# Kernel tuning notes

Measured on AMD Instinct MI355X. Metric: run time of the kernel, lower is better.

The kernel has to match this reference:

```python
import jax, jax.numpy as jnp
import numpy as np

CHUNK = 32
D_INNER, D_STATE, DT_RANK = 512, 16, 32
B_SZ, L_SEQ = 1, 4096


def _chunked_scan(A_bar, Bu, C, cs=CHUNK):
    # A_bar, Bu: (B, L, D, N); C: (B, L, N)
    Bs, L, D, N = A_bar.shape
    pad = (-L) % cs
    if pad:
        A_bar = jnp.pad(A_bar, ((0, 0), (0, pad), (0, 0), (0, 0)), constant_values=1.0)
        Bu = jnp.pad(Bu, ((0, 0), (0, pad), (0, 0), (0, 0)))
        C = jnp.pad(C, ((0, 0), (0, pad), (0, 0)))
    Lp = L + pad
    nc = Lp // cs
    A_c = A_bar.reshape(Bs, nc, cs, D, N)
    Bu_c = Bu.reshape(Bs, nc, cs, D, N)
    C_c = C.reshape(Bs, nc, cs, N)
    # intra-chunk parallel prefix (log-space cumprod)
    A_cum = jnp.exp(jnp.cumsum(jnp.log(jnp.clip(A_c, 1e-8)), axis=2))
    h_intra = A_cum * jnp.cumsum(Bu_c / jnp.clip(A_cum, 1e-8), axis=2)
    total_A = A_cum[:, :, -1]   # (B, nc, D, N)
    h_last = h_intra[:, :, -1]  # (B, nc, D, N)

    def step(carry, inp):
        tA, hL = inp
        return tA * carry + hL, carry  # emit carry BEFORE update (carry_prev)

    init = jnp.zeros((Bs, D, N), A_bar.dtype)
    _, carry_prev = jax.lax.scan(step, init, (jnp.swapaxes(total_A, 0, 1), jnp.swapaxes(h_last, 0, 1)))
    carry_prev = jnp.swapaxes(carry_prev, 0, 1)  # (B, nc, D, N)
    h_full = h_intra + A_cum * carry_prev[:, :, None]
    y = jnp.einsum('bctdn,bctn->bctd', h_full, C_c).reshape(Bs, Lp, D)
    return y[:, :L]


def _chunked_scan_momentum(A_bar, Bu, C, beta, alpha, cs=CHUNK):
    # v_t = beta*v_{t-1} + alpha*Bu_t  resolved via geometric cumsum trick
    L = A_bar.shape[1]
    powers = jnp.arange(L, dtype=Bu.dtype)
    beta_pow = beta ** powers
    Bu_scaled = alpha * Bu / jnp.clip(beta_pow, 1e-12)[None, :, None, None]
    v_series = beta_pow[None, :, None, None] * jnp.cumsum(Bu_scaled, axis=1)
    return _chunked_scan(A_bar, v_series, C, cs)


def setup_inputs() -> dict:
    key = jax.random.key(0)
    ks = jax.random.split(key, 5)
    x = jax.random.normal(ks[0], (B_SZ, L_SEQ, D_INNER), dtype=jnp.float32)
    W_xp = jax.random.normal(ks[1], (DT_RANK + 2 * D_STATE, D_INNER), dtype=jnp.float32) * 0.02
    W_dt = jax.random.normal(ks[2], (D_INNER, DT_RANK), dtype=jnp.float32) * 0.05
    # torch dt bias init: dt ~ exp(U(log1e-3, log1e-1)); bias = log(exp(dt)-1)
    u = jax.random.uniform(ks[3], (D_INNER,), dtype=jnp.float32)
    dt_init = jnp.exp(u * (np.log(0.1) - np.log(0.001)) + np.log(0.001))
    b_dt = jnp.log(jnp.expm1(dt_init))
    A_log = jnp.broadcast_to(jnp.log(jnp.arange(1, D_STATE + 1, dtype=jnp.float32))[None, :], (D_INNER, D_STATE)).copy()
    D_param = jnp.ones((D_INNER,), dtype=jnp.float32)
    alpha = jnp.float32(0.6)
    beta_logit = jnp.float32(np.log(0.99 / (1.0 - 0.99 + 1e-8)))
    return {"x": x, "W_xp": W_xp, "W_dt": W_dt, "b_dt": b_dt, "A_log": A_log,
            "D_param": D_param, "alpha": alpha, "beta_logit": beta_logit}


def reference(x, W_xp, W_dt, b_dt, A_log, D_param, alpha, beta_logit):
    # x: (B, L, d_inner)
    proj = x @ W_xp.T                                   # (B, L, dt_rank + 2N)
    dt_in, Bp, Cp = jnp.split(proj, [DT_RANK, DT_RANK + D_STATE], axis=-1)
    dt = jax.nn.softplus(dt_in @ W_dt.T + b_dt)          # (B, L, D)
    A = -jnp.exp(A_log)                                  # (D, N)
    A_bar = jnp.exp(dt[..., None] * A[None, None])       # (B, L, D, N)
    Bu = dt[..., None] * Bp[:, :, None, :] * x[..., None]  # (B, L, D, N)
    beta = jax.nn.sigmoid(beta_logit)
    y = _chunked_scan_momentum(A_bar, Bu, Cp, beta, alpha, CHUNK)
    return y + D_param * x
```

## Files before the change

kernel.cpp:

```cpp
#include <hip/hip_runtime.h>
#include <math.h>

#define L_SEQ   4096
#define D_INNER 512
#define D_STATE 16
#define DT_RANK 32
#define CHUNK   32
#define NCHUNK  128
#define NCH     8192
#define LN_1EM8 -18.420681f

__global__ __launch_bounds__(256) void k1_proj(
    const float* __restrict__ x, const float* __restrict__ W_xp,
    const float* __restrict__ W_dt, const float* __restrict__ b_dt,
    float* __restrict__ dt_out, float* __restrict__ Bp, float* __restrict__ Cp)
{
    __shared__ __align__(16) float xs[32][36];
    __shared__ __align__(16) float wsd[64][36];
    __shared__ __align__(16) float dtin[32][36];

    const int tid = threadIdx.x;
    const int t0  = blockIdx.x * 32;

    float acc[2][4] = {{0.f,0.f,0.f,0.f},{0.f,0.f,0.f,0.f}};
    const int rt = (tid & 15) * 2;
    const int ct = (tid >> 4) * 4;

    for (int kc = 0; kc < D_INNER; kc += 32) {
        {
            int r  = tid >> 3;
            int k4 = (tid & 7) << 2;
            *(float4*)&xs[r][k4] =
                *(const float4*)&x[(size_t)(t0 + r) * D_INNER + kc + k4];
        }
        #pragma unroll
        for (int i = 0; i < 2; ++i) {
            int e   = tid + i * 256;
            int ccw = e >> 3;
            int kw  = (e & 7) << 2;
            *(float4*)&wsd[ccw][kw] =
                *(const float4*)&W_xp[(size_t)ccw * D_INNER + kc + kw];
        }
        __syncthreads();

        #pragma unroll
        for (int k = 0; k < 32; k += 4) {
            float4 x0 = *(const float4*)&xs[rt][k];
            float4 x1 = *(const float4*)&xs[rt + 1][k];
            float4 w0 = *(const float4*)&wsd[ct][k];
            float4 w1 = *(const float4*)&wsd[ct + 1][k];
            float4 w2 = *(const float4*)&wsd[ct + 2][k];
            float4 w3 = *(const float4*)&wsd[ct + 3][k];
            acc[0][0] += x0.x*w0.x + x0.y*w0.y + x0.z*w0.z + x0.w*w0.w;
            acc[0][1] += x0.x*w1.x + x0.y*w1.y + x0.z*w1.z + x0.w*w1.w;
            acc[0][2] += x0.x*w2.x + x0.y*w2.y + x0.z*w2.z + x0.w*w2.w;
            acc[0][3] += x0.x*w3.x + x0.y*w3.y + x0.z*w3.z + x0.w*w3.w;
            acc[1][0] += x1.x*w0.x + x1.y*w0.y + x1.z*w0.z + x1.w*w0.w;
            acc[1][1] += x1.x*w1.x + x1.y*w1.y + x1.z*w1.z + x1.w*w1.w;
            acc[1][2] += x1.x*w2.x + x1.y*w2.y + x1.z*w2.z + x1.w*w2.w;
            acc[1][3] += x1.x*w3.x + x1.y*w3.y + x1.z*w3.z + x1.w*w3.w;
        }
        __syncthreads();
    }

    #pragma unroll
    for (int rr = 0; rr < 2; ++rr) {
        #pragma unroll
        for (int cj = 0; cj < 4; ++cj) {
            int cc = ct + cj, r = rt + rr;
            float a = acc[rr][cj];
            if (cc < DT_RANK)               dtin[r][cc] = a;
            else if (cc < DT_RANK + D_STATE) Bp[(size_t)(t0 + r) * D_STATE + (cc - DT_RANK)] = a;
            else                             Cp[(size_t)(t0 + r) * D_STATE + (cc - DT_RANK - D_STATE)] = a;
        }
    }
    __syncthreads();

    const int dA = tid * 2, dB = tid * 2 + 1;
    float4 wa[8], wb[8];
    #pragma unroll
    for (int q = 0; q < 8; ++q) {
        wa[q] = *(const float4*)&W_dt[(size_t)dA * DT_RANK + q * 4];
        wb[q] = *(const float4*)&W_dt[(size_t)dB * DT_RANK + q * 4];
    }
    const float bA = b_dt[dA], bB = b_dt[dB];
    for (int r = 0; r < 32; ++r) {
        float zA = bA, zB = bB;
        #pragma unroll
        for (int q = 0; q < 8; ++q) {
            float4 dn = *(const float4*)&dtin[r][q * 4];
            zA += dn.x*wa[q].x + dn.y*wa[q].y + dn.z*wa[q].z + dn.w*wa[q].w;
            zB += dn.x*wb[q].x + dn.y*wb[q].y + dn.z*wb[q].z + dn.w*wb[q].w;
        }
        float2 o;
        o.x = fmaxf(zA, 0.f) + log1pf(expf(-fabsf(zA)));
        o.y = fmaxf(zB, 0.f) + log1pf(expf(-fabsf(zB)));
        *(float2*)&dt_out[(size_t)(t0 + r) * D_INNER + dA] = o;
    }
}

__global__ __launch_bounds__(256) void k2a(
    const float* __restrict__ x, const float* __restrict__ dt,
    const float* __restrict__ Bp, const float* __restrict__ A_log,
    const float* __restrict__ alpha_p, const float* __restrict__ beta_logit_p,
    float4* __restrict__ GTUW)
{
    __shared__ __align__(16) float xs_t[16][36], dts_t[16][36], Bs_t[16][36];
    __shared__ __align__(16) float bpw[32], aib[32];
    const int tid = threadIdx.x;
    const int c   = blockIdx.x;
    const int d0  = blockIdx.y * 16;

    #pragma unroll
    for (int i = 0; i < 2; ++i) {
        int e = tid + i * 256;
        int t = e >> 4, q = e & 15;
        xs_t [q][t] = x [(size_t)(c * CHUNK + t) * D_INNER + d0 + q];
        dts_t[q][t] = dt[(size_t)(c * CHUNK + t) * D_INNER + d0 + q];
        Bs_t [q][t] = Bp[(size_t)(c * CHUNK + t) * D_STATE + q];
    }
    if (tid < CHUNK) {
        float betaf = 1.f / (1.f + expf(-beta_logit_p[0]));
        double lb = log((double)betaf);
        float bp = (float)exp((double)(c * CHUNK + tid) * lb);
        bpw[tid] = bp;
        aib[tid] = alpha_p[0] / fmaxf(bp, 1e-12f);
    }
    __syncthreads();

    const int dl = tid >> 4, n = tid & 15;
    const float A = -expf(A_log[(d0 + dl) * D_STATE + n]);

    float LS = 0.f, csum = 0.f, P1 = 0.f, P2 = 0.f;
    #pragma unroll
    for (int j = 0; j < CHUNK; j += 4) {
        float4 dt4 = *(const float4*)&dts_t[dl][j];
        float4 xx4 = *(const float4*)&xs_t [dl][j];
        float4 BB4 = *(const float4*)&Bs_t [n][j];
        float4 bp4 = *(const float4*)&bpw[j];
        float4 ai4 = *(const float4*)&aib[j];
        #pragma unroll
        for (int u = 0; u < 4; ++u) {
            float dtv = ((const float*)&dt4)[u];
            float xv  = ((const float*)&xx4)[u];
            float Bv  = ((const float*)&BB4)[u];
            float bp  = ((const float*)&bp4)[u];
            float ai  = ((const float*)&ai4)[u];
            float Bu  = dtv * Bv * xv;
            LS   = fmaf(ai, Bu, LS);
            csum = fmaf(dtv, A, csum);
            float rA = (csum < LN_1EM8) ? 1e8f : __expf(-csum);
            float t1 = bp * rA;
            P1 = fmaf(t1, LS, P1);
            P2 += t1;
        }
    }
    float TA = __expf(csum);
    float4 o; o.x = LS; o.y = TA; o.z = TA * P1; o.w = TA * P2;
    GTUW[(size_t)c * NCH + d0 * D_STATE + tid] = o;
}

__global__ __launch_bounds__(64) void k2b(
    const float4* __restrict__ GTUW, float2* __restrict__ SC)
{
    const int ch = blockIdx.x * 64 + threadIdx.x;
    double Soff = 0.0, carry = 0.0;
    for (int c = 0; c < NCHUNK; ++c) {
        const size_t idx = (size_t)c * NCH + ch;
        float2 sc; sc.x = (float)Soff; sc.y = (float)carry;
        SC[idx] = sc;
        float4 g = GTUW[idx];
        carry = (double)g.y * carry + (double)g.z + Soff * (double)g.w;
        Soff += (double)g.x;
    }
}

__global__ __launch_bounds__(256) void k2c(
    const float* __restrict__ x, const float* __restrict__ dt,
    const float* __restrict__ Bp, const float* __restrict__ Cp,
    const float* __restrict__ A_log, const float* __restrict__ D_param,
    const float* __restrict__ alpha_p, const float* __restrict__ beta_logit_p,
    const float2* __restrict__ SC, float* __restrict__ out)
{
    __shared__ __align__(16) float xs_t[16][36], dts_t[16][36];
    __shared__ __align__(16) float Bs_t[16][36], Cs_t[16][36];
    __shared__ __align__(16) float bpw[32], aib[32];
    __shared__ __align__(16) float ys2[CHUNK * 16][20];
    const int tid = threadIdx.x;
    const int c   = blockIdx.x;
    const int d0  = blockIdx.y * 16;

    #pragma unroll
    for (int i = 0; i < 2; ++i) {
        int e = tid + i * 256;
        int t = e >> 4, q = e & 15;
        xs_t [q][t] = x [(size_t)(c * CHUNK + t) * D_INNER + d0 + q];
        dts_t[q][t] = dt[(size_t)(c * CHUNK + t) * D_INNER + d0 + q];
        Bs_t [q][t] = Bp[(size_t)(c * CHUNK + t) * D_STATE + q];
        Cs_t [q][t] = Cp[(size_t)(c * CHUNK + t) * D_STATE + q];
    }
    if (tid < CHUNK) {
        float betaf = 1.f / (1.f + expf(-beta_logit_p[0]));
        double lb = log((double)betaf);
        float bp = (float)exp((double)(c * CHUNK + tid) * lb);
        bpw[tid] = bp;
        aib[tid] = alpha_p[0] / fmaxf(bp, 1e-12f);
    }
    __syncthreads();

    const int dl = tid >> 4, n = tid & 15;
    const float A = -expf(A_log[(d0 + dl) * D_STATE + n]);

    float2 sc = SC[(size_t)c * NCH + d0 * D_STATE + tid];
    const float Soff = sc.x, cprev = sc.y;

    float LS = 0.f, csum = 0.f, P = 0.f;
    #pragma unroll
    for (int j = 0; j < CHUNK; j += 4) {
        float4 dt4 = *(const float4*)&dts_t[dl][j];
        float4 xx4 = *(const float4*)&xs_t [dl][j];
        float4 BB4 = *(const float4*)&Bs_t [n][j];
        float4 CC4 = *(const float4*)&Cs_t [n][j];
        float4 bp4 = *(const float4*)&bpw[j];
        float4 ai4 = *(const float4*)&aib[j];
        #pragma unroll
        for (int u = 0; u < 4; ++u) {
            float dtv = ((const float*)&dt4)[u];
            float xv  = ((const float*)&xx4)[u];
            float Bv  = ((const float*)&BB4)[u];
            float Cv  = ((const float*)&CC4)[u];
            float bp  = ((const float*)&bp4)[u];
            float ai  = ((const float*)&ai4)[u];
            float Bu  = dtv * Bv * xv;
            LS   = fmaf(ai, Bu, LS);
            float v = bp * (Soff + LS);
            csum = fmaf(dtv, A, csum);
            float Acum = __expf(csum);
            float rA = (csum < LN_1EM8) ? 1e8f : __expf(-csum);
            P = fmaf(v, rA, P);
            float hf = Acum * (P + cprev);
            ys2[(j + u) * 16 + dl][n] = hf * Cv;
        }
    }
    __syncthreads();

    #pragma unroll
    for (int i = 0; i < 2; ++i) {
        int p  = tid + i * 256;
        int j  = p >> 4, dl2 = p & 15;
        const float* row = ys2[p];
        float4 a0 = ((const float4*)row)[0];
        float4 a1 = ((const float4*)row)[1];
        float4 a2 = ((const float4*)row)[2];
        float4 a3 = ((const float4*)row)[3];
        float s = a0.x+a0.y+a0.z+a0.w + a1.x+a1.y+a1.z+a1.w
                + a2.x+a2.y+a2.z+a2.w + a3.x+a3.y+a3.z+a3.w;
        int gd = d0 + dl2;
        out[(size_t)(c * CHUNK + j) * D_INNER + gd] = s + D_param[gd] * xs_t[dl2][j];
    }
}

extern "C" void kernel_launch(void* const* d_in, const int* in_sizes, int n_in,
                              void* d_out, int out_size, void* d_ws, size_t ws_size,
                              hipStream_t stream)
{
    const float* x          = (const float*)d_in[0];
    const float* W_xp       = (const float*)d_in[1];
    const float* W_dt       = (const float*)d_in[2];
    const float* b_dt       = (const float*)d_in[3];
    const float* A_log      = (const float*)d_in[4];
    const float* D_param    = (const float*)d_in[5];
    const float* alpha      = (const float*)d_in[6];
    const float* beta_logit = (const float*)d_in[7];
    float* out = (float*)d_out;

    float* ws = (float*)d_ws;
    float*  dt   = ws;
    float*  Bp   = dt + (size_t)L_SEQ * D_INNER;
    float*  Cp   = Bp + (size_t)L_SEQ * D_STATE;
    float4* GTUW = (float4*)(Cp + (size_t)L_SEQ * D_STATE);
    float2* SC   = (float2*)((float*)GTUW + (size_t)4 * NCHUNK * NCH);

    k1_proj<<<L_SEQ / 32, 256, 0, stream>>>(x, W_xp, W_dt, b_dt, dt, Bp, Cp);
    k2a<<<dim3(NCHUNK, D_INNER / 16), 256, 0, stream>>>(
        x, dt, Bp, A_log, alpha, beta_logit, GTUW);
    k2b<<<NCH / 64, 64, 0, stream>>>(GTUW, SC);
    k2c<<<dim3(NCHUNK, D_INNER / 16), 256, 0, stream>>>(
        x, dt, Bp, Cp, A_log, D_param, alpha, beta_logit, SC, out);
}
```

Measured before the change: 169.2 us.

## Split-K projection GEMM, widen scan tiles, prefetch carry scan, shuffle-reduce output

The projection is split into a split-K GEMM over 8 K-slices with a 4x4 register tile, followed by a reduction kernel that also computes dt, B and C. The scan kernels now handle 64 channels per block with 4 states per thread, coalesced row loads and a shuffle reduction over states, instead of a large shared staging buffer. The sequential carry kernel prefetches GTUW four chunks ahead to hide load latency. The cost is one extra launch and a partial-sum buffer that shares workspace with SC, plus fewer blocks in the scan kernels.

```diff
diff --git a/kernel.cpp b/kernel.cpp
--- a/kernel.cpp
+++ b/kernel.cpp
@@ -10,71 +10,81 @@
 #define NCH     8192
 #define LN_1EM8 -18.420681f
 
-__global__ __launch_bounds__(256) void k1_proj(
+__global__ __launch_bounds__(256) void k1a(
     const float* __restrict__ x, const float* __restrict__ W_xp,
-    const float* __restrict__ W_dt, const float* __restrict__ b_dt,
-    float* __restrict__ dt_out, float* __restrict__ Bp, float* __restrict__ Cp)
-{
-    __shared__ __align__(16) float xs[32][36];
-    __shared__ __align__(16) float wsd[64][36];
-    __shared__ __align__(16) float dtin[32][36];
-
+    float* __restrict__ proj_part)
+{
+    __shared__ __align__(16) float xs_t[64][68];
+    __shared__ __align__(16) float ws_t[64][68];
     const int tid = threadIdx.x;
-    const int t0  = blockIdx.x * 32;
-
-    float acc[2][4] = {{0.f,0.f,0.f,0.f},{0.f,0.f,0.f,0.f}};
-    const int rt = (tid & 15) * 2;
-    const int ct = (tid >> 4) * 4;
-
-    for (int kc = 0; kc < D_INNER; kc += 32) {
-        {
-            int r  = tid >> 3;
-            int k4 = (tid & 7) << 2;
-            *(float4*)&xs[r][k4] =
-                *(const float4*)&x[(size_t)(t0 + r) * D_INNER + kc + k4];
+    const int t0  = blockIdx.x * 64;
+    const int k0  = blockIdx.y * 64;
+
+    #pragma unroll
+    for (int i = 0; i < 4; ++i) {
+        int e = tid + i * 256;
+        int r = e >> 4, k4 = (e & 15) << 2;
+        float4 v = *(const float4*)&x[(size_t)(t0 + r) * D_INNER + k0 + k4];
+        xs_t[k4 + 0][r] = v.x; xs_t[k4 + 1][r] = v.y;
+        xs_t[k4 + 2][r] = v.z; xs_t[k4 + 3][r] = v.w;
+        float4 w = *(const float4*)&W_xp[(size_t)r * D_INNER + k0 + k4];
+        ws_t[k4 + 0][r] = w.x; ws_t[k4 + 1][r] = w.y;
+        ws_t[k4 + 2][r] = w.z; ws_t[k4 + 3][r] = w.w;
+    }
+    __syncthreads();
+
+    const int tr = (tid & 15) << 2;
+    const int tc = (tid >> 4) << 2;
+    float a00=0,a01=0,a02=0,a03=0, a10=0,a11=0,a12=0,a13=0;
+    float a20=0,a21=0,a22=0,a23=0, a30=0,a31=0,a32=0,a33=0;
+
+    #pragma unroll 4
+    for (int k = 0; k < 64; ++k) {
+        float4 xv = *(const float4*)&xs_t[k][tr];
+        float4 wv = *(const float4*)&ws_t[k][tc];
+        a00 = fmaf(xv.x, wv.x, a00); a01 = fmaf(xv.x, wv.y, a01);
+        a02 = fmaf(xv.x, wv.z, a02); a03 = fmaf(xv.x, wv.w, a03);
+        a10 = fmaf(xv.y, wv.x, a10); a11 = fmaf(xv.y, wv.y, a11);
+        a12 = fmaf(xv.y, wv.z, a12); a13 = fmaf(xv.y, wv.w, a13);
+        a20 = fmaf(xv.z, wv.x, a20); a21 = fmaf(xv.z, wv.y, a21);
+        a22 = fmaf(xv.z, wv.z, a22); a23 = fmaf(xv.z, wv.w, a23);
+        a30 = fmaf(xv.w, wv.x, a30); a31 = fmaf(xv.w, wv.y, a31);
+        a32 = fmaf(xv.w, wv.z, a32); a33 = fmaf(xv.w, wv.w, a33);
+    }
+    float* base = proj_part + (size_t)blockIdx.y * (L_SEQ * 64);
+    float4 o;
+    o.x=a00; o.y=a01; o.z=a02; o.w=a03; *(float4*)&base[(t0+tr+0)*64 + tc] = o;
+    o.x=a10; o.y=a11; o.z=a12; o.w=a13; *(float4*)&base[(t0+tr+1)*64 + tc] = o;
+    o.x=a20; o.y=a21; o.z=a22; o.w=a23; *(float4*)&base[(t0+tr+2)*64 + tc] = o;
+    o.x=a30; o.y=a31; o.z=a32; o.w=a33; *(float4*)&base[(t0+tr+3)*64 + tc] = o;
+}
+
+__global__ __launch_bounds__(256) void k1b(
+    const float* __restrict__ proj_part, const float* __restrict__ W_dt,
+    const float* __restrict__ b_dt, float* __restrict__ dt_out,
+    float* __restrict__ Bp, float* __restrict__ Cp)
+{
+    __shared__ __align__(16) float ps[16][68];
+    const int tid = threadIdx.x;
+    const int t0  = blockIdx.x * 16;
+
+    {
+        const int r = tid >> 4, q = (tid & 15) << 2;
+        float4 s = {0.f, 0.f, 0.f, 0.f};
+        #pragma unroll
+        for (int p = 0; p < 8; ++p) {
+            float4 v = *(const float4*)&proj_part[(size_t)p * (L_SEQ * 64) + (t0 + r) * 64 + q];
+            s.x += v.x; s.y += v.y; s.z += v.z; s.w += v.w;
         }
-        #pragma unroll
-        for (int i = 0; i < 2; ++i) {
-            int e   = tid + i * 256;
-            int ccw = e >> 3;
-            int kw  = (e & 7) << 2;
-            *(float4*)&wsd[ccw][kw] =
-                *(const float4*)&W_xp[(size_t)ccw * D_INNER + kc + kw];
-        }
-        __syncthreads();
-
-        #pragma unroll
-        for (int k = 0; k < 32; k += 4) {
-            float4 x0 = *(const float4*)&xs[rt][k];
-            float4 x1 = *(const float4*)&xs[rt + 1][k];
-            float4 w0 = *(const float4*)&wsd[ct][k];
-            float4 w1 = *(const float4*)&wsd[ct + 1][k];
-            float4 w2 = *(const float4*)&wsd[ct + 2][k];
-            float4 w3 = *(const float4*)&wsd[ct + 3][k];
-            acc[0][0] += x0.x*w0.x + x0.y*w0.y + x0.z*w0.z + x0.w*w0.w;
-            acc[0][1] += x0.x*w1.x + x0.y*w1.y + x0.z*w1.z + x0.w*w1.w;
-            acc[0][2] += x0.x*w2.x + x0.y*w2.y + x0.z*w2.z + x0.w*w2.w;
-            acc[0][3] += x0.x*w3.x + x0.y*w3.y + x0.z*w3.z + x0.w*w3.w;
-            acc[1][0] += x1.x*w0.x + x1.y*w0.y + x1.z*w0.z + x1.w*w0.w;
-            acc[1][1] += x1.x*w1.x + x1.y*w1.y + x1.z*w1.z + x1.w*w1.w;
-            acc[1][2] += x1.x*w2.x + x1.y*w2.y + x1.z*w2.z + x1.w*w2.w;
-            acc[1][3] += x1.x*w3.x + x1.y*w3.y + x1.z*w3.z + x1.w*w3.w;
-        }
-        __syncthreads();
-    }
-
-    #pragma unroll
-    for (int rr = 0; rr < 2; ++rr) {
-        #pragma unroll
-        for (int cj = 0; cj < 4; ++cj) {
-            int cc = ct + cj, r = rt + rr;
-            float a = acc[rr][cj];
-            if (cc < DT_RANK)               dtin[r][cc] = a;
-            else if (cc < DT_RANK + D_STATE) Bp[(size_t)(t0 + r) * D_STATE + (cc - DT_RANK)] = a;
-            else                             Cp[(size_t)(t0 + r) * D_STATE + (cc - DT_RANK - D_STATE)] = a;
-        }
-    }
-    __syncthreads();
+        *(float4*)&ps[r][q] = s;
+    }
+    __syncthreads();
+
+    {
+        const int r = tid >> 4, n = tid & 15;
+        Bp[(size_t)(t0 + r) * D_STATE + n] = ps[r][32 + n];
+        Cp[(size_t)(t0 + r) * D_STATE + n] = ps[r][48 + n];
+    }
 
     const int dA = tid * 2, dB = tid * 2 + 1;
     float4 wa[8], wb[8];
@@ -84,11 +94,11 @@
         wb[q] = *(const float4*)&W_dt[(size_t)dB * DT_RANK + q * 4];
     }
     const float bA = b_dt[dA], bB = b_dt[dB];
-    for (int r = 0; r < 32; ++r) {
+    for (int r = 0; r < 16; ++r) {
         float zA = bA, zB = bB;
         #pragma unroll
         for (int q = 0; q < 8; ++q) {
-            float4 dn = *(const float4*)&dtin[r][q * 4];
+            float4 dn = *(const float4*)&ps[r][q * 4];
             zA += dn.x*wa[q].x + dn.y*wa[q].y + dn.z*wa[q].z + dn.w*wa[q].w;
             zB += dn.x*wb[q].x + dn.y*wb[q].y + dn.z*wb[q].z + dn.w*wb[q].w;
         }
@@ -105,19 +115,25 @@
     const float* __restrict__ alpha_p, const float* __restrict__ beta_logit_p,
     float4* __restrict__ GTUW)
 {
-    __shared__ __align__(16) float xs_t[16][36], dts_t[16][36], Bs_t[16][36];
-    __shared__ __align__(16) float bpw[32], aib[32];
+    __shared__ float xs[CHUNK][65], dts[CHUNK][65];
+    __shared__ __align__(16) float Bs[CHUNK][20];
+    __shared__ float bpw[CHUNK], aib[CHUNK];
     const int tid = threadIdx.x;
     const int c   = blockIdx.x;
-    const int d0  = blockIdx.y * 16;
-
+    const int d0  = blockIdx.y * 64;
+
+    #pragma unroll
+    for (int i = 0; i < 8; ++i) {
+        int e = tid + i * 256;
+        int t = e >> 6, dl = e & 63;
+        xs [t][dl] = x [(size_t)(c * CHUNK + t) * D_INNER + d0 + dl];
+        dts[t][dl] = dt[(size_t)(c * CHUNK + t) * D_INNER + d0 + dl];
+    }
     #pragma unroll
     for (int i = 0; i < 2; ++i) {
         int e = tid + i * 256;
-        int t = e >> 4, q = e & 15;
-        xs_t [q][t] = x [(size_t)(c * CHUNK + t) * D_INNER + d0 + q];
-        dts_t[q][t] = dt[(size_t)(c * CHUNK + t) * D_INNER + d0 + q];
-        Bs_t [q][t] = Bp[(size_t)(c * CHUNK + t) * D_STATE + q];
+        int t = e >> 4, n = e & 15;
+        Bs[t][n] = Bp[(size_t)(c * CHUNK + t) * D_STATE + n];
     }
     if (tid < CHUNK) {
         float betaf = 1.f / (1.f + expf(-beta_logit_p[0]));
@@ -128,36 +144,37 @@
     }
     __syncthreads();
 
-    const int dl = tid >> 4, n = tid & 15;
-    const float A = -expf(A_log[(d0 + dl) * D_STATE + n]);
-
-    float LS = 0.f, csum = 0.f, P1 = 0.f, P2 = 0.f;
-    #pragma unroll
-    for (int j = 0; j < CHUNK; j += 4) {
-        float4 dt4 = *(const float4*)&dts_t[dl][j];
-        float4 xx4 = *(const float4*)&xs_t [dl][j];
-        float4 BB4 = *(const float4*)&Bs_t [n][j];
-        float4 bp4 = *(const float4*)&bpw[j];
-        float4 ai4 = *(const float4*)&aib[j];
+    const int dl = tid >> 2, n0 = (tid & 3) << 2;
+    float A[4], LS[4] = {0,0,0,0}, cs[4] = {0,0,0,0};
+    float P1[4] = {0,0,0,0}, P2[4] = {0,0,0,0};
+    #pragma unroll
+    for (int i = 0; i < 4; ++i)
+        A[i] = -expf(A_log[(size_t)(d0 + dl) * D_STATE + n0 + i]);
+
+    #pragma unroll 4
+    for (int j = 0; j < CHUNK; ++j) {
+        float dtv = dts[j][dl];
+        float xv  = xs[j][dl];
+        float bp  = bpw[j];
+        float ai  = aib[j];
+        float4 Bv = *(const float4*)&Bs[j][n0];
         #pragma unroll
-        for (int u = 0; u < 4; ++u) {
-            float dtv = ((const float*)&dt4)[u];
-            float xv  = ((const float*)&xx4)[u];
-            float Bv  = ((const float*)&BB4)[u];
-            float bp  = ((const float*)&bp4)[u];
-            float ai  = ((const float*)&ai4)[u];
-            float Bu  = dtv * Bv * xv;
-            LS   = fmaf(ai, Bu, LS);
-            csum = fmaf(dtv, A, csum);
-            float rA = (csum < LN_1EM8) ? 1e8f : __expf(-csum);
+        for (int i = 0; i < 4; ++i) {
+            float Bu = dtv * ((const float*)&Bv)[i] * xv;
+            LS[i] = fmaf(ai, Bu, LS[i]);
+            cs[i] = fmaf(dtv, A[i], cs[i]);
+            float rA = (cs[i] < LN_1EM8) ? 1e8f : __expf(-cs[i]);
             float t1 = bp * rA;
-            P1 = fmaf(t1, LS, P1);
-            P2 += t1;
+            P1[i] = fmaf(t1, LS[i], P1[i]);
+            P2[i] += t1;
         }
     }
-    float TA = __expf(csum);
-    float4 o; o.x = LS; o.y = TA; o.z = TA * P1; o.w = TA * P2;
-    GTUW[(size_t)c * NCH + d0 * D_STATE + tid] = o;
+    #pragma unroll
+    for (int i = 0; i < 4; ++i) {
+        float TA = __expf(cs[i]);
+        float4 o; o.x = LS[i]; o.y = TA; o.z = TA * P1[i]; o.w = TA * P2[i];
+        GTUW[(size_t)c * NCH + (d0 + dl) * D_STATE + n0 + i] = o;
+    }
 }
 
 __global__ __launch_bounds__(64) void k2b(
@@ -165,11 +182,15 @@
 {
     const int ch = blockIdx.x * 64 + threadIdx.x;
     double Soff = 0.0, carry = 0.0;
+    float4 buf[4];
+    #pragma unroll
+    for (int p = 0; p < 4; ++p) buf[p] = GTUW[(size_t)p * NCH + ch];
+    #pragma unroll 4
     for (int c = 0; c < NCHUNK; ++c) {
-        const size_t idx = (size_t)c * NCH + ch;
+        float4 g = buf[c & 3];
+        if (c + 4 < NCHUNK) buf[c & 3] = GTUW[(size_t)(c + 4) * NCH + ch];
         float2 sc; sc.x = (float)Soff; sc.y = (float)carry;
-        SC[idx] = sc;
-        float4 g = GTUW[idx];
+        SC[(size_t)c * NCH + ch] = sc;
         carry = (double)g.y * carry + (double)g.z + Soff * (double)g.w;
         Soff += (double)g.x;
     }
@@ -182,22 +203,27 @@
     const float* __restrict__ alpha_p, const float* __restrict__ beta_logit_p,
     const float2* __restrict__ SC, float* __restrict__ out)
 {
-    __shared__ __align__(16) float xs_t[16][36], dts_t[16][36];
-    __shared__ __align__(16) float Bs_t[16][36], Cs_t[16][36];
-    __shared__ __align__(16) float bpw[32], aib[32];
-    __shared__ __align__(16) float ys2[CHUNK * 16][20];
+    __shared__ float xs[CHUNK][65], dts[CHUNK][65];
+    __shared__ __align__(16) float Bs[CHUNK][20], Cs[CHUNK][20];
+    __shared__ float bpw[CHUNK], aib[CHUNK];
+    __shared__ float ys[CHUNK][65];
     const int tid = threadIdx.x;
     const int c   = blockIdx.x;
-    const int d0  = blockIdx.y * 16;
-
+    const int d0  = blockIdx.y * 64;
+
+    #pragma unroll
+    for (int i = 0; i < 8; ++i) {
+        int e = tid + i * 256;
+        int t = e >> 6, dl = e & 63;
+        xs [t][dl] = x [(size_t)(c * CHUNK + t) * D_INNER + d0 + dl];
+        dts[t][dl] = dt[(size_t)(c * CHUNK + t) * D_INNER + d0 + dl];
+    }
     #pragma unroll
     for (int i = 0; i < 2; ++i) {
         int e = tid + i * 256;
-        int t = e >> 4, q = e & 15;
-        xs_t [q][t] = x [(size_t)(c * CHUNK + t) * D_INNER + d0 + q];
-        dts_t[q][t] = dt[(size_t)(c * CHUNK + t) * D_INNER + d0 + q];
-        Bs_t [q][t] = Bp[(size_t)(c * CHUNK + t) * D_STATE + q];
-        Cs_t [q][t] = Cp[(size_t)(c * CHUNK + t) * D_STATE + q];
+        int t = e >> 4, n = e & 15;
+        Bs[t][n] = Bp[(size_t)(c * CHUNK + t) * D_STATE + n];
+        Cs[t][n] = Cp[(size_t)(c * CHUNK + t) * D_STATE + n];
     }
     if (tid < CHUNK) {
         float betaf = 1.f / (1.f + expf(-beta_logit_p[0]));
@@ -208,55 +234,51 @@
     }
     __syncthreads();
 
-    const int dl = tid >> 4, n = tid & 15;
-    const float A = -expf(A_log[(d0 + dl) * D_STATE + n]);
-
-    float2 sc = SC[(size_t)c * NCH + d0 * D_STATE + tid];
-    const float Soff = sc.x, cprev = sc.y;
-
-    float LS = 0.f, csum = 0.f, P = 0.f;
-    #pragma unroll
-    for (int j = 0; j < CHUNK; j += 4) {
-        float4 dt4 = *(const float4*)&dts_t[dl][j];
-        float4 xx4 = *(const float4*)&xs_t [dl][j];
-        float4 BB4 = *(const float4*)&Bs_t [n][j];
-        float4 CC4 = *(const float4*)&Cs_t [n][j];
-        float4 bp4 = *(const float4*)&bpw[j];
-        float4 ai4 = *(const float4*)&aib[j];
+    const int dl = tid >> 2, n0 = (tid & 3) << 2;
+    float A[4], LS[4] = {0,0,0,0}, cs[4] = {0,0,0,0}, P[4] = {0,0,0,0};
+    float So[4], Cv0[4];
+    #pragma unroll
+    for (int i = 0; i < 4; ++i)
+        A[i] = -expf(A_log[(size_t)(d0 + dl) * D_STATE + n0 + i]);
+    #pragma unroll
+    for (int i = 0; i < 4; ++i) {
+        float2 sc = SC[(size_t)c * NCH + (d0 + dl) * D_STATE + n0 + i];
+        So[i] = sc.x; Cv0[i] = sc.y;
+    }
+
+    #pragma unroll 4
+    for (int j = 0; j < CHUNK; ++j) {
+        float dtv = dts[j][dl];
+        float xv  = xs[j][dl];
+        float bp  = bpw[j];
+        float ai  = aib[j];
+        float4 Bv = *(const float4*)&Bs[j][n0];
+        float4 Cv = *(const float4*)&Cs[j][n0];
+        float contrib = 0.f;
         #pragma unroll
-        for (int u = 0; u < 4; ++u) {
-            float dtv = ((const float*)&dt4)[u];
-            float xv  = ((const float*)&xx4)[u];
-            float Bv  = ((const float*)&BB4)[u];
-            float Cv  = ((const float*)&CC4)[u];
-            float bp  = ((const float*)&bp4)[u];
-            float ai  = ((const float*)&ai4)[u];
-            float Bu  = dtv * Bv * xv;
-            LS   = fmaf(ai, Bu, LS);
-            float v = bp * (Soff + LS);
-            csum = fmaf(dtv, A, csum);
-            float Acum = __expf(csum);
-            float rA = (csum < LN_1EM8) ? 1e8f : __expf(-csum);
-            P = fmaf(v, rA, P);
-            float hf = Acum * (P + cprev);
-            ys2[(j + u) * 16 + dl][n] = hf * Cv;
+        for (int i = 0; i < 4; ++i) {
+            float Bu = dtv * ((const float*)&Bv)[i] * xv;
+            LS[i] = fmaf(ai, Bu, LS[i]);
+            float v = bp * (So[i] + LS[i]);
+            cs[i] = fmaf(dtv, A[i], cs[i]);
+            float Acum = __expf(cs[i]);
+            float rA = (cs[i] < LN_1EM8) ? 1e8f : __expf(-cs[i]);
+            P[i] = fmaf(v, rA, P[i]);
+            float hf = Acum * (P[i] + Cv0[i]);
+            contrib = fmaf(hf, ((const float*)&Cv)[i], contrib);
         }
-    }
-    __syncthreads();
-
-    #pragma unroll
-    for (int i = 0; i < 2; ++i) {
-        int p  = tid + i * 256;
-        int j  = p >> 4, dl2 = p & 15;
-        const float* row = ys2[p];
-        float4 a0 = ((const float4*)row)[0];
-        float4 a1 = ((const float4*)row)[1];
-        float4 a2 = ((const float4*)row)[2];
-        float4 a3 = ((const float4*)row)[3];
-        float s = a0.x+a0.y+a0.z+a0.w + a1.x+a1.y+a1.z+a1.w
-                + a2.x+a2.y+a2.z+a2.w + a3.x+a3.y+a3.z+a3.w;
-        int gd = d0 + dl2;
-        out[(size_t)(c * CHUNK + j) * D_INNER + gd] = s + D_param[gd] * xs_t[dl2][j];
+        contrib += __shfl_xor(contrib, 1);
+        contrib += __shfl_xor(contrib, 2);
+        if ((tid & 3) == 0) ys[j][dl] = contrib;
+    }
+    __syncthreads();
+
+    #pragma unroll
+    for (int i = 0; i < 8; ++i) {
+        int e = tid + i * 256;
+        int t = e >> 6, d2 = e & 63;
+        int gd = d0 + d2;
+        out[(size_t)(c * CHUNK + t) * D_INNER + gd] = ys[t][d2] + D_param[gd] * xs[t][d2];
     }
 }
 
@@ -275,16 +297,19 @@
     float* out = (float*)d_out;
 
     float* ws = (float*)d_ws;
-    float*  dt   = ws;
-    float*  Bp   = dt + (size_t)L_SEQ * D_INNER;
+    float*  dtw  = ws;
+    float*  Bp   = dtw + (size_t)L_SEQ * D_INNER;
     float*  Cp   = Bp + (size_t)L_SEQ * D_STATE;
     float4* GTUW = (float4*)(Cp + (size_t)L_SEQ * D_STATE);
-    float2* SC   = (float2*)((float*)GTUW + (size_t)4 * NCHUNK * NCH);
-
-    k1_proj<<<L_SEQ / 32, 256, 0, stream>>>(x, W_xp, W_dt, b_dt, dt, Bp, Cp);
-    k2a<<<dim3(NCHUNK, D_INNER / 16), 256, 0, stream>>>(
-        x, dt, Bp, A_log, alpha, beta_logit, GTUW);
+    float*  scpp = (float*)GTUW + (size_t)4 * NCHUNK * NCH;
+    float2* SC        = (float2*)scpp;
+    float*  proj_part = scpp;
+
+    k1a<<<dim3(L_SEQ / 64, 8), 256, 0, stream>>>(x, W_xp, proj_part);
+    k1b<<<L_SEQ / 16, 256, 0, stream>>>(proj_part, W_dt, b_dt, dtw, Bp, Cp);
+    k2a<<<dim3(NCHUNK, D_INNER / 64), 256, 0, stream>>>(
+        x, dtw, Bp, A_log, alpha, beta_logit, GTUW);
     k2b<<<NCH / 64, 64, 0, stream>>>(GTUW, SC);
-    k2c<<<dim3(NCHUNK, D_INNER / 16), 256, 0, stream>>>(
-        x, dt, Bp, Cp, A_log, D_param, alpha, beta_logit, SC, out);
-}
+    k2c<<<dim3(NCHUNK, D_INNER / 64), 256, 0, stream>>>(
+        x, dtw, Bp, Cp, A_log, D_param, alpha, beta_logit, SC, out);
+}
```

Result: faster. 157.1 us (-7.2%).
